# Kernel tuning notes

Measured on AMD Instinct MI355X. Metric: run time of the kernel, lower is better.

## Reference

```python
import jax, jax.numpy as jnp
import numpy as np

N, E, DIN, H, DOUT = 100000, 400000, 128, 128, 128
LN_EPS = 1e-5


def _layernorm(x, g, b):
    m = jnp.mean(x, axis=-1, keepdims=True)
    v = jnp.mean((x - m) ** 2, axis=-1, keepdims=True)
    return (x - m) * jax.lax.rsqrt(v + LN_EPS) * g + b


def setup_inputs() -> dict:
    key = jax.random.key(0)
    ks = jax.random.split(key, 24)
    s = 1.0 / np.sqrt(H)
    inp = {
        'feat': jax.random.normal(ks[0], (N, DIN), jnp.float32),
        'edge_src': jax.random.randint(ks[1], (E,), 0, N, jnp.int32),
        'edge_dst': jax.random.randint(ks[2], (E,), 0, N, jnp.int32),
        'W_src': jax.random.normal(ks[3], (DIN, H), jnp.float32) * s,
        'b_src': jax.random.normal(ks[4], (H,), jnp.float32) * s,
        'W_dst': jax.random.normal(ks[5], (DIN, H), jnp.float32) * s,
        'b_dst': jax.random.normal(ks[6], (H,), jnp.float32) * s,
        'W1a': jax.random.normal(ks[7], (H, H), jnp.float32) * s,
        'W1b': jax.random.normal(ks[8], (H, H), jnp.float32) * s,
        'b1': jax.random.normal(ks[9], (H,), jnp.float32) * s,
        'W2': jax.random.normal(ks[10], (H, H), jnp.float32) * s,
        'b2': jax.random.normal(ks[11], (H,), jnp.float32) * s,
        'W3': jax.random.normal(ks[12], (H, H), jnp.float32) * s,
        'b3': jax.random.normal(ks[13], (H,), jnp.float32) * s,
        'ln_g': jnp.ones((H,), jnp.float32),
        'ln_b': jnp.zeros((H,), jnp.float32),
        'Wg1a': jax.random.normal(ks[14], (H, H), jnp.float32) * s,
        'Wg1b': jax.random.normal(ks[15], (H, H), jnp.float32) * s,
        'bg1': jax.random.normal(ks[16], (H,), jnp.float32) * s,
        'Wg2': jax.random.normal(ks[17], (H, 1), jnp.float32) * s,
        'bg2': jax.random.normal(ks[18], (1,), jnp.float32) * s,
        'W_out': jax.random.normal(ks[19], (H, DOUT), jnp.float32) * s,
        'b_out': jax.random.normal(ks[20], (DOUT,), jnp.float32) * s,
    }
    return inp


def reference(feat, edge_src, edge_dst, W_src, b_src, W_dst, b_dst,
              W1a, W1b, b1, W2, b2, W3, b3, ln_g, ln_b,
              Wg1a, Wg1b, bg1, Wg2, bg2, W_out, b_out):
    gelu = lambda x: jax.nn.gelu(x, approximate=False)  # torch nn.GELU default (erf)
    # node-level src/dst transforms, then gather per edge
    src_h = feat @ W_src + b_src                 # [N,H]
    dst_h = feat @ W_dst + b_dst                 # [N,H]
    se = src_h[edge_src]                         # [E,H]
    de = dst_h[edge_dst]                         # [E,H]
    # edge MLP on concat([se,de]) expressed as split weights (same math)
    h = gelu(se @ W1a + de @ W1b + b1)           # [E,H]
    h = gelu(h @ W2 + b2)                        # [E,H]
    msg = _layernorm(h @ W3 + b3, ln_g, ln_b)    # [E,H]
    # message gating
    gate = jax.nn.sigmoid(gelu(se @ Wg1a + de @ Wg1b + bg1) @ Wg2 + bg2)  # [E,1]
    msg = gate * msg
    # scatter-sum to destination nodes, then out transform
    upd = jax.ops.segment_sum(msg, edge_dst, num_segments=N)  # [N,H]
    return upd @ W_out + b_out                   # [N,DOUT]
```

## Files before the change

### kernel.cpp

```cpp
#include <hip/hip_runtime.h>
#include <hip/hip_bf16.h>
#include <math.h>


typedef __bf16 bf16x8 __attribute__((ext_vector_type(8)));
typedef float floatx4 __attribute__((ext_vector_type(4)));

#define LN_EPS 1e-5f

__device__ __forceinline__ unsigned short f2bf(float x) {
  unsigned int u = __float_as_uint(x);
  u = u + 0x7fffu + ((u >> 16) & 1u);
  return (unsigned short)(u >> 16);
}

__device__ __forceinline__ float bf2f(unsigned short s) {
  return __uint_as_float(((unsigned int)s) << 16);
}

__device__ __forceinline__ float geluf(float x) {
  float t = x * x;
  float u = x * (2.3022080f + 0.1029434f * t);
  float e = __builtin_amdgcn_exp2f(-u);
  return x * __builtin_amdgcn_rcpf(1.0f + e);
}

__device__ __forceinline__ float sigmoidf_fast(float x) {
  float e = __builtin_amdgcn_exp2f(-1.44269504f * x);
  return __builtin_amdgcn_rcpf(1.0f + e);
}

__global__ __launch_bounds__(256) void prep_weights(
    const float* w0, const float* w1, const float* w2, const float* w3,
    const float* w4, const float* w5, const float* w6, const float* w7,
    const float* w8, unsigned short* out) {
  const float* srcs[9] = {w0, w1, w2, w3, w4, w5, w6, w7, w8};
  int m = blockIdx.x >> 2, c = blockIdx.x & 3;
  const float* src = srcs[m] + c * 32 * 128;
  __shared__ unsigned short sT[128][35];
  int tid = threadIdx.x;

  for (int it = 0; it < 4; ++it) {
    int f4 = tid + it * 256;
    float4 v = ((const float4*)src)[f4];
    int krel = f4 >> 5;
    int n0 = (f4 & 31) * 4;
    sT[n0 + 0][krel] = f2bf(v.x);
    sT[n0 + 1][krel] = f2bf(v.y);
    sT[n0 + 2][krel] = f2bf(v.z);
    sT[n0 + 3][krel] = f2bf(v.w);
  }
  __syncthreads();
  unsigned short* dst = out + m * 16384 + c * 32;
  for (int it = 0; it < 2; ++it) {
    int ch = tid + it * 256;
    int n = ch >> 2, kc = (ch & 3) * 8;
    unsigned short tmp[8];
    for (int j = 0; j < 8; ++j) tmp[j] = sT[n][kc + j];
    *(int4*)(dst + n * 128 + kc) = *(const int4*)tmp;
  }
}

#define LDB(pB, B)                                              \
  do {                                                          \
    const unsigned short* _p = (pB);                            \
    for (int kb = 0; kb < 4; ++kb) {                            \
      B[0][kb] = *(const bf16x8*)(_p + kb * 32);                \
      B[1][kb] = *(const bf16x8*)(_p + 2048 + kb * 32);         \
    }                                                           \
  } while (0)

__global__ __launch_bounds__(256, 4) void node_fused(
    const float* __restrict__ feat, const unsigned short* __restrict__ wT,
    const float* __restrict__ b_src, const float* __restrict__ b_dst,
    const float* __restrict__ b1, const float* __restrict__ bg1,
    unsigned short* __restrict__ SrcCat, unsigned short* __restrict__ DstCat,
    unsigned short* __restrict__ upd, int M) {
  __shared__ __align__(16) unsigned short sF[64][136];
  __shared__ __align__(16) unsigned short sT[64][136];
  int tid = threadIdx.x;
  int r0 = blockIdx.x * 64;
  int y = blockIdx.y;

  if (y == 0) {
    int4 z = {0, 0, 0, 0};
    int4* p = (int4*)(upd + (long long)r0 * 128);
    for (int it = 0; it < 4; ++it) {
      int idx = tid + it * 256;
      if (r0 + (idx >> 4) < M) p[idx] = z;
    }
  }

  {
    int r = tid >> 2, seg = tid & 3;
    int row = r0 + r;
    const float* src = feat + (long long)row * 128;
    for (int it = 0; it < 4; ++it) {
      int c = (seg * 4 + it) * 8;
      unsigned short tmp[8];
      if (row < M) {
        float4 f0 = *(const float4*)(src + c);
        float4 f1 = *(const float4*)(src + c + 4);
        tmp[0] = f2bf(f0.x); tmp[1] = f2bf(f0.y); tmp[2] = f2bf(f0.z); tmp[3] = f2bf(f0.w);
        tmp[4] = f2bf(f1.x); tmp[5] = f2bf(f1.y); tmp[6] = f2bf(f1.z); tmp[7] = f2bf(f1.w);
      } else {
        for (int j = 0; j < 8; ++j) tmp[j] = 0;
      }
      *(int4*)&sF[r][c] = *(const int4*)tmp;
    }
  }
  __syncthreads();

  int w = tid >> 6, lane = tid & 63, lr = lane & 15, q = lane >> 4;
  int c0 = 32 * w + lr, c1 = 32 * w + 16 + lr;
  const unsigned short* pB = wT + c0 * 128 + q * 8;

  const unsigned short* wH = pB + (y ? 1 : 0) * 16384;
  const unsigned short* wA = pB + (y ? 3 : 2) * 16384;
  const unsigned short* wG = pB + (y ? 7 : 6) * 16384;
  unsigned short* Cat = y ? DstCat : SrcCat;
  float hb0 = y ? b_dst[c0] : b_src[c0];
  float hb1 = y ? b_dst[c1] : b_src[c1];
  float ab0 = y ? 0.f : b1[c0];
  float ab1 = y ? 0.f : b1[c1];
  float gb0 = y ? 0.f : bg1[c0];
  float gb1 = y ? 0.f : bg1[c1];

  bf16x8 B[2][4];

  auto pass = [&](const unsigned short (*Ab)[136], floatx4 (&acc)[4][2]) {
    for (int kb = 0; kb < 4; ++kb) {
      int k = kb * 32 + q * 8;
      for (int mb = 0; mb < 4; ++mb) {
        bf16x8 a = *(const bf16x8*)&Ab[16 * mb + lr][k];
        acc[mb][0] = __builtin_amdgcn_mfma_f32_16x16x32_bf16(a, B[0][kb], acc[mb][0], 0, 0, 0);
        acc[mb][1] = __builtin_amdgcn_mfma_f32_16x16x32_bf16(a, B[1][kb], acc[mb][1], 0, 0, 0);
      }
    }
  };

  {
    floatx4 acc[4][2];
    for (int mb = 0; mb < 4; ++mb)
      for (int nb = 0; nb < 2; ++nb) acc[mb][nb] = (floatx4){0.f, 0.f, 0.f, 0.f};
    LDB(wH, B);
    pass(sF, acc);
    for (int mb = 0; mb < 4; ++mb)
      for (int i = 0; i < 4; ++i) {
        int r = 16 * mb + 4 * q + i;
        sT[r][c0] = f2bf(acc[mb][0][i] + hb0);
        sT[r][c1] = f2bf(acc[mb][1][i] + hb1);
      }
  }
  __syncthreads();

  floatx4 accA[4][2], accP[4][2];
  for (int mb = 0; mb < 4; ++mb)
    for (int nb = 0; nb < 2; ++nb) {
      accA[mb][nb] = (floatx4){0.f, 0.f, 0.f, 0.f};
      accP[mb][nb] = (floatx4){0.f, 0.f, 0.f, 0.f};
    }
  LDB(wA, B);
  pass(sT, accA);
  LDB(wG, B);
  pass(sT, accP);
  __syncthreads();

  for (int mb = 0; mb < 4; ++mb)
    for (int i = 0; i < 4; ++i) {
      int r = 16 * mb + 4 * q + i;
      sF[r][c0] = f2bf(accA[mb][0][i] + ab0);
      sF[r][c1] = f2bf(accA[mb][1][i] + ab1);
      sT[r][c0] = f2bf(accP[mb][0][i] + gb0);
      sT[r][c1] = f2bf(accP[mb][1][i] + gb1);
    }
  __syncthreads();

  for (int it = 0; it < 8; ++it) {
    int idx = tid + it * 256;
    int row = idx >> 5, c = idx & 31;
    if (r0 + row < M) {
      const void* src = (c < 16) ? (const void*)&sF[row][c * 8]
                                 : (const void*)&sT[row][(c - 16) * 8];
      *(int4*)(Cat + (long long)(r0 + row) * 256 + c * 8) = *(const int4*)src;
    }
  }
}

__global__ __launch_bounds__(256, 4) void gemm_out(
    const unsigned short* __restrict__ A, const unsigned short* __restrict__ Bt,
    const float* __restrict__ bias, float* __restrict__ C, int M) {
  __shared__ __align__(16) char smem[64 * 130 * 4];
  unsigned short (*sA)[136] = (unsigned short(*)[136])smem;
  float (*sO)[130] = (float(*)[130])smem;
  int tid = threadIdx.x;
  int r0 = blockIdx.x * 64;

  {
    int r = tid >> 2, seg = tid & 3;
    int row = r0 + r;
    const int4* src = (const int4*)(A + (long long)row * 128);
    for (int it = 0; it < 4; ++it) {
      int c = seg * 4 + it;
      int4 v;
      if (row < M) v = src[c];
      else v = (int4){0, 0, 0, 0};
      *(int4*)&sA[r][c * 8] = v;
    }
  }
  __syncthreads();

  int w = tid >> 6, lane = tid & 63, lr = lane & 15, q = lane >> 4;
  int c0 = 32 * w + lr, c1 = 32 * w + 16 + lr;
  const unsigned short* pB = Bt + c0 * 128 + q * 8;

  bf16x8 B[2][4];
  LDB(pB, B);
  floatx4 acc[4][2];
  for (int mb = 0; mb < 4; ++mb)
    for (int nb = 0; nb < 2; ++nb) acc[mb][nb] = (floatx4){0.f, 0.f, 0.f, 0.f};
  for (int kb = 0; kb < 4; ++kb) {
    int k = kb * 32 + q * 8;
    for (int mb = 0; mb < 4; ++mb) {
      bf16x8 a = *(const bf16x8*)&sA[16 * mb + lr][k];
      acc[mb][0] = __builtin_amdgcn_mfma_f32_16x16x32_bf16(a, B[0][kb], acc[mb][0], 0, 0, 0);
      acc[mb][1] = __builtin_amdgcn_mfma_f32_16x16x32_bf16(a, B[1][kb], acc[mb][1], 0, 0, 0);
    }
  }
  __syncthreads();

  float bv0 = bias[c0], bv1 = bias[c1];
  for (int mb = 0; mb < 4; ++mb)
    for (int i = 0; i < 4; ++i) {
      int r = 16 * mb + 4 * q + i;
      sO[r][c0] = acc[mb][0][i] + bv0;
      sO[r][c1] = acc[mb][1][i] + bv1;
    }
  __syncthreads();

  for (int it = 0; it < 8; ++it) {
    int idx = tid + it * 256;
    int row = idx >> 5, c = idx & 31;
    if (r0 + row < M)
      *(float4*)(C + (long long)(r0 + row) * 128 + c * 4) = *(const float4*)&sO[row][c * 4];
  }
}

__global__ __launch_bounds__(256, 6) void edge_fused(
    const unsigned short* __restrict__ SrcCat, const unsigned short* __restrict__ DstCat,
    const int* __restrict__ edge_src, const int* __restrict__ edge_dst,
    const unsigned short* __restrict__ wT,
    const float* __restrict__ b2, const float* __restrict__ b3,
    const float* __restrict__ ln_g, const float* __restrict__ ln_b,
    const float* __restrict__ Wg2, const float* __restrict__ bg2,
    unsigned short* __restrict__ upd, int E) {
  __shared__ __align__(16) unsigned short sH[64][136];
  __shared__ int sDst[64];
  __shared__ float sGate[64];
  __shared__ float sR1[4][64];
  __shared__ float sR2[4][64];
  __shared__ float sM[64];
  __shared__ float sRS[64];

  int tid = threadIdx.x;
  int e0 = blockIdx.x * 64;

  {
    int r = tid >> 2, seg = tid & 3;
    int e = e0 + r;
    int ee = (e < E) ? e : (E - 1);
    int es = edge_src[ee], ed = edge_dst[ee];
    if (seg == 0) sDst[r] = (e < E) ? ed : -1;
    const unsigned short* ps = SrcCat + (long long)es * 256 + seg * 32;
    const unsigned short* pd = DstCat + (long long)ed * 256 + seg * 32;

    int4 sa[4], sb[4], ga[4], gb[4];
    for (int u = 0; u < 4; ++u) {
      sa[u] = ((const int4*)ps)[u];
      sb[u] = ((const int4*)pd)[u];
      ga[u] = ((const int4*)(ps + 128))[u];
      gb[u] = ((const int4*)(pd + 128))[u];
    }
    for (int u = 0; u < 4; ++u) {
      const unsigned short* av = (const unsigned short*)&sa[u];
      const unsigned short* bv = (const unsigned short*)&sb[u];
      unsigned short outv[8];
      for (int j = 0; j < 8; ++j)
        outv[j] = f2bf(geluf(bf2f(av[j]) + bf2f(bv[j])));
      *(int4*)&sH[r][seg * 32 + u * 8] = *(const int4*)outv;
    }
    float gp = 0.f;
    for (int u = 0; u < 4; ++u) {
      const unsigned short* av = (const unsigned short*)&ga[u];
      const unsigned short* bv = (const unsigned short*)&gb[u];
      float4 w0 = *(const float4*)(Wg2 + seg * 32 + u * 8);
      float4 w1 = *(const float4*)(Wg2 + seg * 32 + u * 8 + 4);
      gp += geluf(bf2f(av[0]) + bf2f(bv[0])) * w0.x;
      gp += geluf(bf2f(av[1]) + bf2f(bv[1])) * w0.y;
      gp += geluf(bf2f(av[2]) + bf2f(bv[2])) * w0.z;
      gp += geluf(bf2f(av[3]) + bf2f(bv[3])) * w0.w;
      gp += geluf(bf2f(av[4]) + bf2f(bv[4])) * w1.x;
      gp += geluf(bf2f(av[5]) + bf2f(bv[5])) * w1.y;
      gp += geluf(bf2f(av[6]) + bf2f(bv[6])) * w1.z;
      gp += geluf(bf2f(av[7]) + bf2f(bv[7])) * w1.w;
    }
    gp += __shfl_xor(gp, 1);
    gp += __shfl_xor(gp, 2);
    if (seg == 0) sGate[r] = sigmoidf_fast(gp + bg2[0]);
  }
  __syncthreads();

  int w = tid >> 6, lane = tid & 63, lr = lane & 15, q = lane >> 4;
  int c0 = 32 * w + lr, c1 = 32 * w + 16 + lr;
  const unsigned short* pB = wT + c0 * 128 + q * 8;

  bf16x8 B[2][4];
  floatx4 acc[4][2];
  auto zacc = [&]() {
    for (int mb = 0; mb < 4; ++mb)
      for (int nb = 0; nb < 2; ++nb) acc[mb][nb] = (floatx4){0.f, 0.f, 0.f, 0.f};
  };
  auto pass = [&](const unsigned short (*Ab)[136]) {
    for (int kb = 0; kb < 4; ++kb) {
      int k = kb * 32 + q * 8;
      for (int mb = 0; mb < 4; ++mb) {
        bf16x8 a = *(const bf16x8*)&Ab[16 * mb + lr][k];
        acc[mb][0] = __builtin_amdgcn_mfma_f32_16x16x32_bf16(a, B[0][kb], acc[mb][0], 0, 0, 0);
        acc[mb][1] = __builtin_amdgcn_mfma_f32_16x16x32_bf16(a, B[1][kb], acc[mb][1], 0, 0, 0);
      }
    }
  };

  LDB(pB + 4 * 16384, B);
  zacc();
  pass(sH);
  __syncthreads();
  {
    float bv0 = b2[c0], bv1 = b2[c1];
    for (int mb = 0; mb < 4; ++mb)
      for (int i = 0; i < 4; ++i) {
        int r = 16 * mb + 4 * q + i;
        sH[r][c0] = f2bf(geluf(acc[mb][0][i] + bv0));
        sH[r][c1] = f2bf(geluf(acc[mb][1][i] + bv1));
      }
  }
  __syncthreads();

  LDB(pB + 5 * 16384, B);
  zacc();
  pass(sH);
  {
    float bv0 = b3[c0], bv1 = b3[c1];
    for (int mb = 0; mb < 4; ++mb)
      for (int i = 0; i < 4; ++i) {
        float x0 = acc[mb][0][i] + bv0;
        float x1 = acc[mb][1][i] + bv1;
        acc[mb][0][i] = x0; acc[mb][1][i] = x1;
        float s = x0 + x1, s2 = x0 * x0 + x1 * x1;
        s += __shfl_xor(s, 1); s += __shfl_xor(s, 2);
        s += __shfl_xor(s, 4); s += __shfl_xor(s, 8);
        s2 += __shfl_xor(s2, 1); s2 += __shfl_xor(s2, 2);
        s2 += __shfl_xor(s2, 4); s2 += __shfl_xor(s2, 8);
        if (lr == 0) { sR1[w][16 * mb + 4 * q + i] = s; sR2[w][16 * mb + 4 * q + i] = s2; }
      }
  }
  __syncthreads();
  if (tid < 64) {
    float s = sR1[0][tid] + sR1[1][tid] + sR1[2][tid] + sR1[3][tid];
    float s2 = sR2[0][tid] + sR2[1][tid] + sR2[2][tid] + sR2[3][tid];
    float m = s * (1.f / 128.f);
    float v = s2 * (1.f / 128.f) - m * m;
    sM[tid] = m;
    sRS[tid] = rsqrtf(v + LN_EPS);
  }
  __syncthreads();

  {
    float lg0 = ln_g[c0], lg1 = ln_g[c1];
    float lb0 = ln_b[c0], lb1 = ln_b[c1];
    for (int mb = 0; mb < 4; ++mb)
      for (int i = 0; i < 4; ++i) {
        int r = 16 * mb + 4 * q + i;
        int dst = sDst[r];
        float m = sM[r], rs = sRS[r], gt = sGate[r];
        float v0 = ((acc[mb][0][i] - m) * rs * lg0 + lb0) * gt;
        float v1 = ((acc[mb][1][i] - m) * rs * lg1 + lb1) * gt;
        float o0 = __shfl_xor(v0, 1);
        float o1 = __shfl_xor(v1, 1);
        if (dst >= 0) {
          unsigned int pk;
          int colb;
          if ((lr & 1) == 0) {
            pk = (unsigned int)f2bf(v0) | ((unsigned int)f2bf(o0) << 16);
            colb = c0;
          } else {
            pk = (unsigned int)f2bf(o1) | ((unsigned int)f2bf(v1) << 16);
            colb = c0 + 15;
          }
          unsigned short* addr = upd + (long long)dst * 128 + colb;
          asm volatile("global_atomic_pk_add_bf16 %0, %1, off"
                       :: "v"(addr), "v"(pk) : "memory");
        }
      }
  }
}

extern "C" void kernel_launch(void* const* d_in, const int* in_sizes, int n_in,
                              void* d_out, int out_size, void* d_ws, size_t ws_size,
                              hipStream_t stream) {
  const float* feat   = (const float*)d_in[0];
  const int* edge_src = (const int*)d_in[1];
  const int* edge_dst = (const int*)d_in[2];
  const float* W_src = (const float*)d_in[3];  const float* b_src = (const float*)d_in[4];
  const float* W_dst = (const float*)d_in[5];  const float* b_dst = (const float*)d_in[6];
  const float* W1a = (const float*)d_in[7];    const float* W1b = (const float*)d_in[8];
  const float* b1  = (const float*)d_in[9];
  const float* W2  = (const float*)d_in[10];   const float* b2  = (const float*)d_in[11];
  const float* W3  = (const float*)d_in[12];   const float* b3  = (const float*)d_in[13];
  const float* ln_g = (const float*)d_in[14];  const float* ln_b = (const float*)d_in[15];
  const float* Wg1a = (const float*)d_in[16];  const float* Wg1b = (const float*)d_in[17];
  const float* bg1  = (const float*)d_in[18];
  const float* Wg2  = (const float*)d_in[19];  const float* bg2 = (const float*)d_in[20];
  const float* W_out = (const float*)d_in[21]; const float* b_out = (const float*)d_in[22];

  int N = in_sizes[0] / 128;
  int E = in_sizes[1];

  char* ws = (char*)d_ws;
  unsigned short* wT = (unsigned short*)ws;
  size_t off = 9 * 16384 * sizeof(unsigned short);
  unsigned short* SrcCat = (unsigned short*)(ws + off);
  off += (size_t)N * 256 * sizeof(unsigned short);
  unsigned short* DstCat = (unsigned short*)(ws + off);
  off += (size_t)N * 256 * sizeof(unsigned short);
  unsigned short* upd = (unsigned short*)(ws + off);

  prep_weights<<<36, 256, 0, stream>>>(W_src, W_dst, W1a, W1b, W2, W3, Wg1a, Wg1b,
                                       W_out, wT);
  int mtiles = (N + 63) / 64;
  node_fused<<<dim3(mtiles, 2), 256, 0, stream>>>(feat, wT, b_src, b_dst, b1, bg1,
                                                  SrcCat, DstCat, upd, N);
  edge_fused<<<(E + 63) / 64, 256, 0, stream>>>(SrcCat, DstCat, edge_src, edge_dst,
                                                wT, b2, b3, ln_g, ln_b, Wg2, bg2,
                                                upd, E);
  gemm_out<<<mtiles, 256, 0, stream>>>(upd, wT + 8 * 16384, b_out, (float*)d_out, N);
}
```

Baseline: 369.3 us.

## Halve node tile rows to 32 and use packed hardware bf16 conversion

The node_fused and gemm_out kernels now process 32 rows per block instead of 64, with smaller shared buffers and accumulators and launch bounds raised from 4 to 6 blocks per CU. This gives twice as many blocks and more occupancy for the node-level GEMMs. Separately, the manual bit-twiddling float-to-bf16 rounding is replaced with a packed two-value conversion via __bf16 casts, which may map to a native packed convert instruction, in both node and edge kernels. The cost is that each block loads the weights again per 32 rows instead of per 64 rows, so weight traffic per row doubles.

```diff
diff --git a/kernel.cpp b/kernel.cpp
--- a/kernel.cpp
+++ b/kernel.cpp
@@ -4,6 +4,7 @@
 
 
 typedef __bf16 bf16x8 __attribute__((ext_vector_type(8)));
+typedef __bf16 bf16x2 __attribute__((ext_vector_type(2)));
 typedef float floatx4 __attribute__((ext_vector_type(4)));
 
 #define LN_EPS 1e-5f
@@ -12,6 +13,13 @@
   unsigned int u = __float_as_uint(x);
   u = u + 0x7fffu + ((u >> 16) & 1u);
   return (unsigned short)(u >> 16);
+}
+
+__device__ __forceinline__ unsigned int pkbf(float lo, float hi) {
+  bf16x2 v;
+  v.x = (__bf16)lo;
+  v.y = (__bf16)hi;
+  return __builtin_bit_cast(unsigned int, v);
 }
 
 __device__ __forceinline__ float bf2f(unsigned short s) {
@@ -70,49 +78,48 @@
     }                                                           \
   } while (0)
 
-__global__ __launch_bounds__(256, 4) void node_fused(
+__global__ __launch_bounds__(256, 6) void node_fused(
     const float* __restrict__ feat, const unsigned short* __restrict__ wT,
     const float* __restrict__ b_src, const float* __restrict__ b_dst,
     const float* __restrict__ b1, const float* __restrict__ bg1,
     unsigned short* __restrict__ SrcCat, unsigned short* __restrict__ DstCat,
     unsigned short* __restrict__ upd, int M) {
-  __shared__ __align__(16) unsigned short sF[64][136];
-  __shared__ __align__(16) unsigned short sT[64][136];
+  __shared__ __align__(16) unsigned short sF[32][136];
+  __shared__ __align__(16) unsigned short sT[32][136];
   int tid = threadIdx.x;
-  int r0 = blockIdx.x * 64;
+  int r0 = blockIdx.x * 32;
   int y = blockIdx.y;
 
   if (y == 0) {
     int4 z = {0, 0, 0, 0};
     int4* p = (int4*)(upd + (long long)r0 * 128);
-    for (int it = 0; it < 4; ++it) {
+    for (int it = 0; it < 2; ++it) {
       int idx = tid + it * 256;
       if (r0 + (idx >> 4) < M) p[idx] = z;
     }
   }
 
   {
-    int r = tid >> 2, seg = tid & 3;
+    int r = tid >> 3, seg = tid & 7;
     int row = r0 + r;
-    const float* src = feat + (long long)row * 128;
-    for (int it = 0; it < 4; ++it) {
-      int c = (seg * 4 + it) * 8;
-      unsigned short tmp[8];
-      if (row < M) {
-        float4 f0 = *(const float4*)(src + c);
-        float4 f1 = *(const float4*)(src + c + 4);
-        tmp[0] = f2bf(f0.x); tmp[1] = f2bf(f0.y); tmp[2] = f2bf(f0.z); tmp[3] = f2bf(f0.w);
-        tmp[4] = f2bf(f1.x); tmp[5] = f2bf(f1.y); tmp[6] = f2bf(f1.z); tmp[7] = f2bf(f1.w);
-      } else {
-        for (int j = 0; j < 8; ++j) tmp[j] = 0;
-      }
-      *(int4*)&sF[r][c] = *(const int4*)tmp;
-    }
+    const float* src = feat + (long long)row * 128 + seg * 16;
+    unsigned int tmp[8];
+    if (row < M) {
+      for (int j = 0; j < 4; ++j) {
+        float4 f = *(const float4*)(src + j * 4);
+        tmp[2 * j]     = pkbf(f.x, f.y);
+        tmp[2 * j + 1] = pkbf(f.z, f.w);
+      }
+    } else {
+      for (int j = 0; j < 8; ++j) tmp[j] = 0;
+    }
+    *(int4*)&sF[r][seg * 16]     = *(const int4*)&tmp[0];
+    *(int4*)&sF[r][seg * 16 + 8] = *(const int4*)&tmp[4];
   }
   __syncthreads();
 
   int w = tid >> 6, lane = tid & 63, lr = lane & 15, q = lane >> 4;
-  int c0 = 32 * w + lr, c1 = 32 * w + 16 + lr;
+  int c0 = 32 * w + lr, c1 = c0 + 16;
   const unsigned short* pB = wT + c0 * 128 + q * 8;
 
   const unsigned short* wH = pB + (y ? 1 : 0) * 16384;
@@ -128,10 +135,10 @@
 
   bf16x8 B[2][4];
 
-  auto pass = [&](const unsigned short (*Ab)[136], floatx4 (&acc)[4][2]) {
+  auto pass = [&](const unsigned short (*Ab)[136], floatx4 (&acc)[2][2]) {
     for (int kb = 0; kb < 4; ++kb) {
       int k = kb * 32 + q * 8;
-      for (int mb = 0; mb < 4; ++mb) {
+      for (int mb = 0; mb < 2; ++mb) {
         bf16x8 a = *(const bf16x8*)&Ab[16 * mb + lr][k];
         acc[mb][0] = __builtin_amdgcn_mfma_f32_16x16x32_bf16(a, B[0][kb], acc[mb][0], 0, 0, 0);
         acc[mb][1] = __builtin_amdgcn_mfma_f32_16x16x32_bf16(a, B[1][kb], acc[mb][1], 0, 0, 0);
@@ -140,22 +147,23 @@
   };
 
   {
-    floatx4 acc[4][2];
-    for (int mb = 0; mb < 4; ++mb)
+    floatx4 acc[2][2];
+    for (int mb = 0; mb < 2; ++mb)
       for (int nb = 0; nb < 2; ++nb) acc[mb][nb] = (floatx4){0.f, 0.f, 0.f, 0.f};
     LDB(wH, B);
     pass(sF, acc);
-    for (int mb = 0; mb < 4; ++mb)
+    for (int mb = 0; mb < 2; ++mb)
       for (int i = 0; i < 4; ++i) {
         int r = 16 * mb + 4 * q + i;
-        sT[r][c0] = f2bf(acc[mb][0][i] + hb0);
-        sT[r][c1] = f2bf(acc[mb][1][i] + hb1);
-      }
-  }
-  __syncthreads();
-
-  floatx4 accA[4][2], accP[4][2];
-  for (int mb = 0; mb < 4; ++mb)
+        unsigned int u = pkbf(acc[mb][0][i] + hb0, acc[mb][1][i] + hb1);
+        sT[r][c0] = (unsigned short)u;
+        sT[r][c1] = (unsigned short)(u >> 16);
+      }
+  }
+  __syncthreads();
+
+  floatx4 accA[2][2], accP[2][2];
+  for (int mb = 0; mb < 2; ++mb)
     for (int nb = 0; nb < 2; ++nb) {
       accA[mb][nb] = (floatx4){0.f, 0.f, 0.f, 0.f};
       accP[mb][nb] = (floatx4){0.f, 0.f, 0.f, 0.f};
@@ -166,17 +174,19 @@
   pass(sT, accP);
   __syncthreads();
 
-  for (int mb = 0; mb < 4; ++mb)
+  for (int mb = 0; mb < 2; ++mb)
     for (int i = 0; i < 4; ++i) {
       int r = 16 * mb + 4 * q + i;
-      sF[r][c0] = f2bf(accA[mb][0][i] + ab0);
-      sF[r][c1] = f2bf(accA[mb][1][i] + ab1);
-      sT[r][c0] = f2bf(accP[mb][0][i] + gb0);
-      sT[r][c1] = f2bf(accP[mb][1][i] + gb1);
-    }
-  __syncthreads();
-
-  for (int it = 0; it < 8; ++it) {
+      unsigned int ua = pkbf(accA[mb][0][i] + ab0, accA[mb][1][i] + ab1);
+      sF[r][c0] = (unsigned short)ua;
+      sF[r][c1] = (unsigned short)(ua >> 16);
+      unsigned int up = pkbf(accP[mb][0][i] + gb0, accP[mb][1][i] + gb1);
+      sT[r][c0] = (unsigned short)up;
+      sT[r][c1] = (unsigned short)(up >> 16);
+    }
+  __syncthreads();
+
+  for (int it = 0; it < 4; ++it) {
     int idx = tid + it * 256;
     int row = idx >> 5, c = idx & 31;
     if (r0 + row < M) {
@@ -187,41 +197,36 @@
   }
 }
 
-__global__ __launch_bounds__(256, 4) void gemm_out(
+__global__ __launch_bounds__(256, 6) void gemm_out(
     const unsigned short* __restrict__ A, const unsigned short* __restrict__ Bt,
     const float* __restrict__ bias, float* __restrict__ C, int M) {
-  __shared__ __align__(16) char smem[64 * 130 * 4];
+  __shared__ __align__(16) char smem[32 * 130 * 4];
   unsigned short (*sA)[136] = (unsigned short(*)[136])smem;
   float (*sO)[130] = (float(*)[130])smem;
   int tid = threadIdx.x;
-  int r0 = blockIdx.x * 64;
-
-  {
-    int r = tid >> 2, seg = tid & 3;
-    int row = r0 + r;
-    const int4* src = (const int4*)(A + (long long)row * 128);
-    for (int it = 0; it < 4; ++it) {
-      int c = seg * 4 + it;
-      int4 v;
-      if (row < M) v = src[c];
-      else v = (int4){0, 0, 0, 0};
-      *(int4*)&sA[r][c * 8] = v;
-    }
+  int r0 = blockIdx.x * 32;
+
+  for (int it = 0; it < 2; ++it) {
+    int idx = tid + it * 256;
+    int row = idx >> 4, c = idx & 15;
+    int4 v = {0, 0, 0, 0};
+    if (r0 + row < M) v = ((const int4*)(A + (long long)(r0 + row) * 128))[c];
+    *(int4*)&sA[row][c * 8] = v;
   }
   __syncthreads();
 
   int w = tid >> 6, lane = tid & 63, lr = lane & 15, q = lane >> 4;
-  int c0 = 32 * w + lr, c1 = 32 * w + 16 + lr;
+  int c0 = 32 * w + lr, c1 = c0 + 16;
   const unsigned short* pB = Bt + c0 * 128 + q * 8;
 
   bf16x8 B[2][4];
   LDB(pB, B);
-  floatx4 acc[4][2];
-  for (int mb = 0; mb < 4; ++mb)
+  floatx4 acc[2][2];
+  for (int mb = 0; mb < 2; ++mb)
     for (int nb = 0; nb < 2; ++nb) acc[mb][nb] = (floatx4){0.f, 0.f, 0.f, 0.f};
   for (int kb = 0; kb < 4; ++kb) {
     int k = kb * 32 + q * 8;
-    for (int mb = 0; mb < 4; ++mb) {
+    for (int mb = 0; mb < 2; ++mb) {
       bf16x8 a = *(const bf16x8*)&sA[16 * mb + lr][k];
       acc[mb][0] = __builtin_amdgcn_mfma_f32_16x16x32_bf16(a, B[0][kb], acc[mb][0], 0, 0, 0);
       acc[mb][1] = __builtin_amdgcn_mfma_f32_16x16x32_bf16(a, B[1][kb], acc[mb][1], 0, 0, 0);
@@ -230,7 +235,7 @@
   __syncthreads();
 
   float bv0 = bias[c0], bv1 = bias[c1];
-  for (int mb = 0; mb < 4; ++mb)
+  for (int mb = 0; mb < 2; ++mb)
     for (int i = 0; i < 4; ++i) {
       int r = 16 * mb + 4 * q + i;
       sO[r][c0] = acc[mb][0][i] + bv0;
@@ -238,7 +243,7 @@
     }
   __syncthreads();
 
-  for (int it = 0; it < 8; ++it) {
+  for (int it = 0; it < 4; ++it) {
     int idx = tid + it * 256;
     int row = idx >> 5, c = idx & 31;
     if (r0 + row < M)
@@ -284,10 +289,13 @@
     for (int u = 0; u < 4; ++u) {
       const unsigned short* av = (const unsigned short*)&sa[u];
       const unsigned short* bv = (const unsigned short*)&sb[u];
-      unsigned short outv[8];
-      for (int j = 0; j < 8; ++j)
-        outv[j] = f2bf(geluf(bf2f(av[j]) + bf2f(bv[j])));
-      *(int4*)&sH[r][seg * 32 + u * 8] = *(const int4*)outv;
+      unsigned int ov[4];
+      for (int j = 0; j < 4; ++j) {
+        float g0 = geluf(bf2f(av[2 * j])     + bf2f(bv[2 * j]));
+        float g1 = geluf(bf2f(av[2 * j + 1]) + bf2f(bv[2 * j + 1]));
+        ov[j] = pkbf(g0, g1);
+      }
+      *(int4*)&sH[r][seg * 32 + u * 8] = *(const int4*)ov;
     }
     float gp = 0.f;
     for (int u = 0; u < 4; ++u) {
@@ -340,8 +348,9 @@
     for (int mb = 0; mb < 4; ++mb)
       for (int i = 0; i < 4; ++i) {
         int r = 16 * mb + 4 * q + i;
-        sH[r][c0] = f2bf(geluf(acc[mb][0][i] + bv0));
-        sH[r][c1] = f2bf(geluf(acc[mb][1][i] + bv1));
+        unsigned int u = pkbf(geluf(acc[mb][0][i] + bv0), geluf(acc[mb][1][i] + bv1));
+        sH[r][c0] = (unsigned short)u;
+        sH[r][c1] = (unsigned short)(u >> 16);
       }
   }
   __syncthreads();
@@ -391,10 +400,10 @@
           unsigned int pk;
           int colb;
           if ((lr & 1) == 0) {
-            pk = (unsigned int)f2bf(v0) | ((unsigned int)f2bf(o0) << 16);
+            pk = pkbf(v0, o0);
             colb = c0;
           } else {
-            pk = (unsigned int)f2bf(o1) | ((unsigned int)f2bf(v1) << 16);
+            pk = pkbf(o1, v1);
             colb = c0 + 15;
           }
           unsigned short* addr = upd + (long long)dst * 128 + colb;
@@ -437,7 +446,7 @@
 
   prep_weights<<<36, 256, 0, stream>>>(W_src, W_dst, W1a, W1b, W2, W3, Wg1a, Wg1b,
                                        W_out, wT);
-  int mtiles = (N + 63) / 64;
+  int mtiles = (N + 31) / 32;
   node_fused<<<dim3(mtiles, 2), 256, 0, stream>>>(feat, wT, b_src, b_dst, b1, bg1,
                                                   SrcCat, DstCat, upd, N);
   edge_fused<<<(E + 63) / 64, 256, 0, stream>>>(SrcCat, DstCat, edge_src, edge_dst,
```

Measured after the change: 383.7 us. 3.9% more time.
